# Optimization experiments

Hardware: AMD Instinct MI355X
Metric: run time of the kernel (lower is better)

## Reference

```python
import jax, jax.numpy as jnp
import numpy as np

NUM_HEADS = 16
NEG_INF = -2.0**32 + 1.0  # matches torch code's padding value
LN_EPS = 1e-5


def setup_inputs() -> dict:
    key = jax.random.key(0)
    ks = jax.random.split(key, 4)
    B, S, D = 8, 1024, 1024
    x = jax.random.normal(ks[0], (B, S, D), dtype=jnp.float32)
    W_qkv = jax.random.normal(ks[1], (D, 3 * D), dtype=jnp.float32) * 0.02
    b_qkv = jnp.zeros((3 * D,), dtype=jnp.float32)
    W_out = jax.random.normal(ks[2], (D, D), dtype=jnp.float32) * 0.02
    b_out = jnp.zeros((D,), dtype=jnp.float32)
    gamma = jnp.ones((D,), dtype=jnp.float32)
    beta = jnp.zeros((D,), dtype=jnp.float32)
    return {"x": x, "W_qkv": W_qkv, "b_qkv": b_qkv, "W_out": W_out,
            "b_out": b_out, "gamma": gamma, "beta": beta}


def reference(x, W_qkv, b_qkv, W_out, b_out, gamma, beta):
    B, S, D = x.shape
    H = NUM_HEADS
    hd = D // H
    # fused QKV projection
    qkv = x @ W_qkv + b_qkv                      # [B, S, 3D]
    q, k, v = jnp.split(qkv, 3, axis=-1)         # each [B, S, D]
    # split heads: chunk along feature dim == reshape to [B, H, S, hd]
    q = q.reshape(B, S, H, hd).transpose(0, 2, 1, 3)
    k = k.reshape(B, S, H, hd).transpose(0, 2, 1, 3)
    v = v.reshape(B, S, H, hd).transpose(0, 2, 1, 3)
    # NOTE: original scales by sqrt(num_units), not sqrt(head_dim)
    scale = jnp.float32(1.0 / (D ** 0.5))
    scores = jnp.einsum('bhqd,bhkd->bhqk', q, k) * scale   # [B, H, S, S]
    causal = jnp.tril(jnp.ones((S, S), dtype=bool))
    scores = jnp.where(causal, scores, jnp.float32(NEG_INF))
    attn = jax.nn.softmax(scores, axis=-1)
    o = jnp.einsum('bhqk,bhkd->bhqd', attn, v)             # [B, H, S, hd]
    o = o.transpose(0, 2, 1, 3).reshape(B, S, D)           # concat heads
    out = o @ W_out + b_out + x                            # proj + residual
    # LayerNorm over last dim
    mu = jnp.mean(out, axis=-1, keepdims=True)
    var = jnp.mean((out - mu) ** 2, axis=-1, keepdims=True)
    out = (out - mu) * jax.lax.rsqrt(var + LN_EPS) * gamma + beta
    return out
```

## Files before the change

kernel.cpp:

```cpp
#include <hip/hip_runtime.h>
#include <math.h>

typedef __attribute__((ext_vector_type(8))) short bf16x8;
typedef __attribute__((ext_vector_type(4))) float f32x4;

#define DEV __device__ __forceinline__

DEV unsigned short f2b(float f) {
    union { float f; unsigned u; } x;
    x.f = f;
    unsigned r = x.u + 0x7fff + ((x.u >> 16) & 1);
    return (unsigned short)(r >> 16);
}
DEV float b2f(unsigned short u) {
    union { unsigned u; float f; } x;
    x.u = ((unsigned)u) << 16;
    return x.f;
}

DEV void glds16(const void* g, void* l) {
    __builtin_amdgcn_global_load_lds(
        (const __attribute__((address_space(1))) void*)g,
        (__attribute__((address_space(3))) void*)l, 16, 0, 0);
}

__global__ __launch_bounds__(256) void cvt_bf16(
    const float* __restrict__ in, unsigned short* __restrict__ out)
{
    int i = (blockIdx.x * 256 + threadIdx.x) * 8;
    float4 a = *(const float4*)(in + i);
    float4 b = *(const float4*)(in + i + 4);
    int4 tv;
    short* tp = reinterpret_cast<short*>(&tv);
    tp[0] = (short)f2b(a.x); tp[1] = (short)f2b(a.y);
    tp[2] = (short)f2b(a.z); tp[3] = (short)f2b(a.w);
    tp[4] = (short)f2b(b.x); tp[5] = (short)f2b(b.y);
    tp[6] = (short)f2b(b.z); tp[7] = (short)f2b(b.w);
    *(int4*)(out + i) = tv;
}

__global__ __launch_bounds__(256) void transpose_cvt(
    const float* __restrict__ W, unsigned short* __restrict__ Wt, int N)
{
    __shared__ short S[64 * 65];
    const int n0 = blockIdx.x * 64, k0 = blockIdx.y * 64;
    const int tid = threadIdx.x;
#pragma unroll
    for (int p = 0; p < 16; p++) {
        int idx = p * 256 + tid;
        int r = idx >> 6, c = idx & 63;
        S[c * 65 + r] = (short)f2b(W[(size_t)(k0 + r) * N + n0 + c]);
    }
    __syncthreads();
#pragma unroll
    for (int p = 0; p < 8; p++) {
        int idx = p * 256 + tid;
        int r = idx >> 5, cp = (idx & 31) * 2;
        unsigned lo = (unsigned short)S[r * 65 + cp];
        unsigned hi = (unsigned short)S[r * 65 + cp + 1];
        *(unsigned*)(Wt + (size_t)(n0 + r) * 1024 + k0 + cp) = lo | (hi << 16);
    }
}

__global__ __launch_bounds__(512, 4) void qkv_gemm(
    const unsigned short* __restrict__ Xb,
    const unsigned short* __restrict__ Wt,
    const float* __restrict__ bq,
    unsigned short* __restrict__ Qb,
    unsigned short* __restrict__ Kf,
    unsigned short* __restrict__ Vf)
{
    __shared__ __align__(16) short As[256 * 64];
    __shared__ __align__(16) short Bs[128 * 64];

    const int flat = blockIdx.y * 24 + blockIdx.x;
    const int xcd = flat & 7, local = flat >> 3;
    const int m0 = (xcd * 4 + local / 24) * 256;
    const int n0 = (local % 24) * 128;

    const int tid = threadIdx.x;
    const int wave = tid >> 6, lane = tid & 63;
    const int quad = lane >> 4, lcol = lane & 15;
    const int wr = wave >> 1, wc = wave & 1;
    const int wrow = wr * 64, wcol = wc * 64;

    f32x4 acc[4][4];
#pragma unroll
    for (int i = 0; i < 4; i++)
#pragma unroll
        for (int j = 0; j < 4; j++) acc[i][j] = (f32x4){0.f, 0.f, 0.f, 0.f};

    const int sr = tid >> 3;
    const int g_lin = tid & 7;
    const int g_src = g_lin ^ (sr & 7);
    const int swz = lcol & 7;

    for (int k0 = 0; k0 < 1024; k0 += 64) {
        __syncthreads();
#pragma unroll
        for (int p = 0; p < 4; p++)
            glds16(Xb + (size_t)(m0 + p * 64 + sr) * 1024 + k0 + g_src * 8,
                   &As[(p * 64 + sr) * 64 + g_lin * 8]);
#pragma unroll
        for (int p = 0; p < 2; p++)
            glds16(Wt + (size_t)(n0 + p * 64 + sr) * 1024 + k0 + g_src * 8,
                   &Bs[(p * 64 + sr) * 64 + g_lin * 8]);
        __syncthreads();
#pragma unroll
        for (int kk = 0; kk < 2; kk++) {
            bf16x8 a[4], b[4];
#pragma unroll
            for (int i = 0; i < 4; i++)
                a[i] = *(const bf16x8*)(&As[(wrow + 16 * i + lcol) * 64
                                            + ((kk * 4 + quad) ^ swz) * 8]);
#pragma unroll
            for (int j = 0; j < 4; j++)
                b[j] = *(const bf16x8*)(&Bs[(wcol + 16 * j + lcol) * 64
                                            + ((kk * 4 + quad) ^ swz) * 8]);
#pragma unroll
            for (int i = 0; i < 4; i++)
#pragma unroll
                for (int j = 0; j < 4; j++)
                    acc[i][j] = __builtin_amdgcn_mfma_f32_16x16x32_bf16(
                        a[i], b[j], acc[i][j], 0, 0, 0);
        }
    }
    __syncthreads();

    short* Es = As;
    const int which = n0 >> 10;
    const int h0 = (n0 & 1023) >> 6;
    const int bb = m0 >> 10;
    const int sl0 = m0 & 1023;

#pragma unroll
    for (int hh = 0; hh < 2; hh++) {
        if ((wr >> 1) == hh) {
#pragma unroll
            for (int j = 0; j < 4; j++) {
                int colt = wcol + 16 * j + lcol;
                float bias = bq[n0 + colt];
                int g = colt >> 6, e = colt & 63;
#pragma unroll
                for (int i = 0; i < 4; i++) {
#pragma unroll
                    for (int reg = 0; reg < 4; reg++) {
                        int ls = (wr & 1) * 64 + 16 * i + quad * 4 + reg;
                        unsigned short v = f2b(acc[i][j][reg] + bias);
                        int off;
                        if (which == 0)
                            off = ls * 64 + e;
                        else if (which == 1)
                            off = (e >> 5) * 4096 + (ls >> 4) * 512
                                + (((e >> 3) & 3) * 16 + (ls & 15)) * 8 + (e & 7);
                        else
                            off = (ls >> 5) * 2048 + (e >> 4) * 512
                                + ((((ls >> 3) & 3) * 16) + (e & 15)) * 8 + (ls & 7);
                        Es[g * 8192 + off] = (short)v;
                    }
                }
            }
        }
        __syncthreads();
        const int kt = (sl0 >> 7) + hh;
#pragma unroll
        for (int rd = 0; rd < 4; rd++) {
            int fl = rd * 4096 + tid * 8;
            int g = fl >> 13, off = fl & 8191;
            bf16x8 val = *(const bf16x8*)(&Es[fl]);
            int bh = bb * 16 + h0 + g;
            if (which == 0)
                *(bf16x8*)(Qb + ((size_t)bh * 1024 + sl0 + hh * 128) * 64 + off) = val;
            else if (which == 1)
                *(bf16x8*)(Kf + ((size_t)bh * 8 + kt) * 8192 + off) = val;
            else
                *(bf16x8*)(Vf + ((size_t)bh * 8 + kt) * 8192 + off) = val;
        }
        if (hh == 0) __syncthreads();
    }
}

__global__ __launch_bounds__(256, 4) void attn_kern(
    const unsigned short* __restrict__ Qb,
    const unsigned short* __restrict__ Kf,
    const unsigned short* __restrict__ Vf,
    unsigned short* __restrict__ Ob)
{
    __shared__ __align__(16) short Ps[64 * 136];

    const int xb = blockIdx.x;
    const int bh = blockIdx.y;
    const int pr = xb >> 1;
    const int hf = xb & 1;
    const unsigned short* Qp = Qb + (size_t)bh * 65536;
    const unsigned short* Kp = Kf + (size_t)bh * 65536;
    const unsigned short* Vp = Vf + (size_t)bh * 65536;

    const int tid = threadIdx.x;
    const int wave = tid >> 6, lane = tid & 63;
    const int quad = lane >> 4, lcol = lane & 15;
    const int hw4 = hf * 4 + wave;
    const int qloc = hw4 * 16 + lcol;

    const float sc2 = 0.0450711882f;
    const int b = bh >> 4, h = bh & 15;

    for (int pass = 0; pass < 2; pass++) {
        const int qt = pass ? (7 - pr) : pr;
        const int q0 = qt * 128 + hf * 64 + wave * 16;

        bf16x8 qa[2];
#pragma unroll
        for (int kk = 0; kk < 2; kk++)
            qa[kk] = *(const bf16x8*)(Qp + (size_t)(q0 + lcol) * 64
                                      + kk * 32 + quad * 8);

        f32x4 o_acc[4];
#pragma unroll
        for (int jo = 0; jo < 4; jo++) o_acc[jo] = (f32x4){0.f, 0.f, 0.f, 0.f};
        float l_loc = 0.f;

        for (int kt = 0; kt <= qt; kt++) {
            const bool diag = (kt == qt);
            const int jmax = diag ? hw4 : 7;
            const int kk2max = diag ? (hw4 >> 1) : 3;

            f32x4 scT[8];
#pragma unroll
            for (int j = 0; j < 8; j++) scT[j] = (f32x4){0.f, 0.f, 0.f, 0.f};
#pragma unroll
            for (int kk = 0; kk < 2; kk++) {
                bf16x8 kb[8];
#pragma unroll
                for (int j = 0; j < 8; j++)
                    if (j <= jmax)
                        kb[j] = *(const bf16x8*)(Kp
                            + ((size_t)((kt * 2 + kk) * 8 + j) << 9) + lane * 8);
#pragma unroll
                for (int j = 0; j < 8; j++)
                    if (j <= jmax)
                        scT[j] = __builtin_amdgcn_mfma_f32_16x16x32_bf16(
                            kb[j], qa[kk], scT[j], 0, 0, 0);
            }

#pragma unroll
            for (int j = 0; j < 8; j++) {
                if (j <= jmax) {
                    float pv[4];
#pragma unroll
                    for (int r = 0; r < 4; r++) {
                        float p = exp2f(scT[j][r] * sc2);
                        if (diag && (16 * j + quad * 4 + r) > qloc) p = 0.f;
                        l_loc += p;
                        pv[r] = p;
                    }
                    ushort4 pk;
                    pk.x = f2b(pv[0]); pk.y = f2b(pv[1]);
                    pk.z = f2b(pv[2]); pk.w = f2b(pv[3]);
                    *(ushort4*)(&Ps[(wave * 16 + lcol) * 136 + 16 * j + quad * 4]) = pk;
                }
            }
            if (diag && !(jmax & 1)) {
                *(ushort4*)(&Ps[(wave * 16 + lcol) * 136 + 16 * (jmax + 1) + quad * 4]) =
                    (ushort4){0, 0, 0, 0};
            }

#pragma unroll
            for (int kk2 = 0; kk2 < 4; kk2++) {
                if (kk2 <= kk2max) {
                    bf16x8 pa = *(const bf16x8*)(&Ps[(wave * 16 + lcol) * 136
                                                     + kk2 * 32 + quad * 8]);
                    bf16x8 vb[4];
#pragma unroll
                    for (int jo = 0; jo < 4; jo++)
                        vb[jo] = *(const bf16x8*)(Vp
                            + ((size_t)((kt * 4 + kk2) * 4 + jo) << 9) + lane * 8);
#pragma unroll
                    for (int jo = 0; jo < 4; jo++)
                        o_acc[jo] = __builtin_amdgcn_mfma_f32_16x16x32_bf16(
                            pa, vb[jo], o_acc[jo], 0, 0, 0);
                }
            }
        }

        l_loc += __shfl_xor(l_loc, 16);
        l_loc += __shfl_xor(l_loc, 32);
        float inv = 1.0f / l_loc;
        float invq[4];
#pragma unroll
        for (int r = 0; r < 4; r++) invq[r] = __shfl(inv, quad * 4 + r);

#pragma unroll
        for (int jo = 0; jo < 4; jo++) {
#pragma unroll
            for (int r = 0; r < 4; r++) {
                int q = q0 + quad * 4 + r;
                Ob[(size_t)(b * 1024 + q) * 1024 + h * 64 + 16 * jo + lcol] =
                    f2b(o_acc[jo][r] * invq[r]);
            }
        }
        l_loc = 0.f;
    }
}

__global__ __launch_bounds__(256) void out_gemm(
    const unsigned short* __restrict__ O,
    const unsigned short* __restrict__ Wt2,
    const float* __restrict__ bo,
    const float* __restrict__ X,
    unsigned short* __restrict__ P2)
{
    __shared__ __align__(16) short As[128 * 64];
    __shared__ __align__(16) short Bs[128 * 64];

    const int flat = blockIdx.y * 8 + blockIdx.x;
    const int xcd = flat & 7, local = flat >> 3;
    const int m0 = (xcd * 8 + (local >> 3)) * 128;
    const int n0 = (local & 7) * 128;

    const int tid = threadIdx.x;
    const int wave = tid >> 6, lane = tid & 63;
    const int quad = lane >> 4, lcol = lane & 15;
    const int wrow = (wave >> 1) * 64, wcol = (wave & 1) * 64;

    f32x4 acc[4][4];
#pragma unroll
    for (int i = 0; i < 4; i++)
#pragma unroll
        for (int j = 0; j < 4; j++) acc[i][j] = (f32x4){0.f, 0.f, 0.f, 0.f};

    const int sr = tid >> 3;
    const int g_lin = tid & 7;
    const int g_src = g_lin ^ (sr & 7);
    const int swz = lcol & 7;

    for (int k0 = 0; k0 < 1024; k0 += 64) {
        __syncthreads();
#pragma unroll
        for (int p = 0; p < 4; p++) {
            glds16(O + (size_t)(m0 + p * 32 + sr) * 1024 + k0 + g_src * 8,
                   &As[(p * 32 + sr) * 64 + g_lin * 8]);
            glds16(Wt2 + (size_t)(n0 + p * 32 + sr) * 1024 + k0 + g_src * 8,
                   &Bs[(p * 32 + sr) * 64 + g_lin * 8]);
        }
        __syncthreads();
#pragma unroll
        for (int kk = 0; kk < 2; kk++) {
            bf16x8 a[4], b[4];
#pragma unroll
            for (int i = 0; i < 4; i++)
                a[i] = *(const bf16x8*)(&As[(wrow + 16 * i + lcol) * 64
                                            + ((kk * 4 + quad) ^ swz) * 8]);
#pragma unroll
            for (int j = 0; j < 4; j++)
                b[j] = *(const bf16x8*)(&Bs[(wcol + 16 * j + lcol) * 64
                                            + ((kk * 4 + quad) ^ swz) * 8]);
#pragma unroll
            for (int i = 0; i < 4; i++)
#pragma unroll
                for (int j = 0; j < 4; j++)
                    acc[i][j] = __builtin_amdgcn_mfma_f32_16x16x32_bf16(
                        a[i], b[j], acc[i][j], 0, 0, 0);
        }
    }

#pragma unroll
    for (int j = 0; j < 4; j++) {
        int c = n0 + wcol + 16 * j + lcol;
        float bias = bo[c];
#pragma unroll
        for (int i = 0; i < 4; i++) {
#pragma unroll
            for (int reg = 0; reg < 4; reg++) {
                int r = m0 + wrow + 16 * i + quad * 4 + reg;
                float v = acc[i][j][reg] + bias + X[(size_t)r * 1024 + c];
                P2[(size_t)r * 1024 + c] = f2b(v);
            }
        }
    }
}

__global__ __launch_bounds__(256) void ln_kern(
    const unsigned short* __restrict__ P2,
    const float* __restrict__ G,
    const float* __restrict__ Bt,
    float* __restrict__ out)
{
    const int row = blockIdx.x, tid = threadIdx.x;
    const size_t base = (size_t)row * 1024 + tid * 4;

    int2 raw = *(const int2*)(P2 + base);
    float v[4];
    v[0] = b2f((unsigned short)(raw.x & 0xffff));
    v[1] = b2f((unsigned short)((unsigned)raw.x >> 16));
    v[2] = b2f((unsigned short)(raw.y & 0xffff));
    v[3] = b2f((unsigned short)((unsigned)raw.y >> 16));

    float sum = v[0] + v[1] + v[2] + v[3];
    float sq = v[0] * v[0] + v[1] * v[1] + v[2] * v[2] + v[3] * v[3];
#pragma unroll
    for (int m = 1; m < 64; m <<= 1) {
        sum += __shfl_xor(sum, m);
        sq += __shfl_xor(sq, m);
    }
    __shared__ float rs[4], rq[4];
    const int wave = tid >> 6, lane = tid & 63;
    if (lane == 0) { rs[wave] = sum; rq[wave] = sq; }
    __syncthreads();
    sum = rs[0] + rs[1] + rs[2] + rs[3];
    sq = rq[0] + rq[1] + rq[2] + rq[3];

    float mean = sum * (1.0f / 1024.0f);
    float var = fmaxf(sq * (1.0f / 1024.0f) - mean * mean, 0.0f);
    float rstd = rsqrtf(var + 1e-5f);

    float4 g = *(const float4*)(G + tid * 4);
    float4 be = *(const float4*)(Bt + tid * 4);

    float4 o;
    o.x = (v[0] - mean) * rstd * g.x + be.x;
    o.y = (v[1] - mean) * rstd * g.y + be.y;
    o.z = (v[2] - mean) * rstd * g.z + be.z;
    o.w = (v[3] - mean) * rstd * g.w + be.w;
    *(float4*)(out + base) = o;
}

extern "C" void kernel_launch(void* const* d_in, const int* in_sizes, int n_in,
                              void* d_out, int out_size, void* d_ws, size_t ws_size,
                              hipStream_t stream) {
    const float* x    = (const float*)d_in[0];
    const float* Wqkv = (const float*)d_in[1];
    const float* bqkv = (const float*)d_in[2];
    const float* Wout = (const float*)d_in[3];
    const float* bout = (const float*)d_in[4];
    const float* gam  = (const float*)d_in[5];
    const float* bet  = (const float*)d_in[6];
    float* out = (float*)d_out;

    char* ws = (char*)d_ws;
    const size_t MB = (size_t)1024 * 1024;

    unsigned short* Qb  = (unsigned short*)d_out;
    unsigned short* Ob  = (unsigned short*)d_out + 8388608;
    unsigned short* Kf  = (unsigned short*)(ws);
    unsigned short* Vf  = (unsigned short*)(ws + 16 * MB);
    unsigned short* Wt2 = (unsigned short*)(ws + 32 * MB);
    unsigned short* Xb  = (unsigned short*)(ws + 34 * MB);
    unsigned short* Wt  = (unsigned short*)(ws + 50 * MB);
    unsigned short* P2  = (unsigned short*)(ws + 34 * MB);

    cvt_bf16<<<4096, 256, 0, stream>>>(x, Xb);
    transpose_cvt<<<dim3(48, 16), 256, 0, stream>>>(Wqkv, Wt, 3072);
    transpose_cvt<<<dim3(16, 16), 256, 0, stream>>>(Wout, Wt2, 1024);
    qkv_gemm<<<dim3(24, 32), 512, 0, stream>>>(Xb, Wt, bqkv, Qb, Kf, Vf);
    attn_kern<<<dim3(8, 128), 256, 0, stream>>>(Qb, Kf, Vf, Ob);
    out_gemm<<<dim3(8, 64), 256, 0, stream>>>(Ob, Wt2, bout, x, P2);
    ln_kern<<<8192, 256, 0, stream>>>(P2, gam, bet, out);
}
```

Baseline: 292.0 us.

## Merge prep kernels into one launch, add MFMA priority hints, relax qkv launch bounds

Folds the input bf16 conversion and both weight transpose-converts into a single prep kernel, dispatching on block index, which saves two kernel launches and their tail gaps. Wraps the MFMA bursts in the attention kernel with s_setprio raise/lower so waves issuing matrix ops are favoured over waves doing softmax and loads. Drops the min-blocks hint from qkv_gemm's launch bounds, so the compiler has more registers to use per thread but occupancy may fall. The prep kernel now has divergent block roles and keeps shared memory allocated even for the conversion blocks.

```diff
diff --git a/kernel.cpp b/kernel.cpp
--- a/kernel.cpp
+++ b/kernel.cpp
@@ -24,27 +24,40 @@
         (__attribute__((address_space(3))) void*)l, 16, 0, 0);
 }
 
-__global__ __launch_bounds__(256) void cvt_bf16(
-    const float* __restrict__ in, unsigned short* __restrict__ out)
-{
-    int i = (blockIdx.x * 256 + threadIdx.x) * 8;
-    float4 a = *(const float4*)(in + i);
-    float4 b = *(const float4*)(in + i + 4);
-    int4 tv;
-    short* tp = reinterpret_cast<short*>(&tv);
-    tp[0] = (short)f2b(a.x); tp[1] = (short)f2b(a.y);
-    tp[2] = (short)f2b(a.z); tp[3] = (short)f2b(a.w);
-    tp[4] = (short)f2b(b.x); tp[5] = (short)f2b(b.y);
-    tp[6] = (short)f2b(b.z); tp[7] = (short)f2b(b.w);
-    *(int4*)(out + i) = tv;
-}
-
-__global__ __launch_bounds__(256) void transpose_cvt(
-    const float* __restrict__ W, unsigned short* __restrict__ Wt, int N)
+__global__ __launch_bounds__(256) void prep_kern(
+    const float* __restrict__ x,    unsigned short* __restrict__ Xb,
+    const float* __restrict__ Wqkv, unsigned short* __restrict__ Wt,
+    const float* __restrict__ Wout, unsigned short* __restrict__ Wt2)
 {
     __shared__ short S[64 * 65];
-    const int n0 = blockIdx.x * 64, k0 = blockIdx.y * 64;
-    const int tid = threadIdx.x;
+    const int id = blockIdx.x, tid = threadIdx.x;
+
+    if (id < 4096) {
+        int i = (id * 256 + tid) * 8;
+        float4 a = *(const float4*)(x + i);
+        float4 b = *(const float4*)(x + i + 4);
+        int4 tv;
+        short* tp = reinterpret_cast<short*>(&tv);
+        tp[0] = (short)f2b(a.x); tp[1] = (short)f2b(a.y);
+        tp[2] = (short)f2b(a.z); tp[3] = (short)f2b(a.w);
+        tp[4] = (short)f2b(b.x); tp[5] = (short)f2b(b.y);
+        tp[6] = (short)f2b(b.z); tp[7] = (short)f2b(b.w);
+        *(int4*)(Xb + i) = tv;
+        return;
+    }
+
+    const float* W;
+    unsigned short* Wo;
+    int N, n0, k0;
+    if (id < 4864) {
+        int t = id - 4096;
+        W = Wqkv; Wo = Wt; N = 3072;
+        n0 = (t % 48) * 64; k0 = (t / 48) * 64;
+    } else {
+        int t = id - 4864;
+        W = Wout; Wo = Wt2; N = 1024;
+        n0 = (t % 16) * 64; k0 = (t / 16) * 64;
+    }
 #pragma unroll
     for (int p = 0; p < 16; p++) {
         int idx = p * 256 + tid;
@@ -58,11 +71,11 @@
         int r = idx >> 5, cp = (idx & 31) * 2;
         unsigned lo = (unsigned short)S[r * 65 + cp];
         unsigned hi = (unsigned short)S[r * 65 + cp + 1];
-        *(unsigned*)(Wt + (size_t)(n0 + r) * 1024 + k0 + cp) = lo | (hi << 16);
-    }
-}
-
-__global__ __launch_bounds__(512, 4) void qkv_gemm(
+        *(unsigned*)(Wo + (size_t)(n0 + r) * 1024 + k0 + cp) = lo | (hi << 16);
+    }
+}
+
+__global__ __launch_bounds__(512) void qkv_gemm(
     const unsigned short* __restrict__ Xb,
     const unsigned short* __restrict__ Wt,
     const float* __restrict__ bq,
@@ -236,11 +249,13 @@
                     if (j <= jmax)
                         kb[j] = *(const bf16x8*)(Kp
                             + ((size_t)((kt * 2 + kk) * 8 + j) << 9) + lane * 8);
+                __builtin_amdgcn_s_setprio(1);
 #pragma unroll
                 for (int j = 0; j < 8; j++)
                     if (j <= jmax)
                         scT[j] = __builtin_amdgcn_mfma_f32_16x16x32_bf16(
                             kb[j], qa[kk], scT[j], 0, 0, 0);
+                __builtin_amdgcn_s_setprio(0);
             }
 
 #pragma unroll
@@ -275,10 +290,12 @@
                     for (int jo = 0; jo < 4; jo++)
                         vb[jo] = *(const bf16x8*)(Vp
                             + ((size_t)((kt * 4 + kk2) * 4 + jo) << 9) + lane * 8);
+                    __builtin_amdgcn_s_setprio(1);
 #pragma unroll
                     for (int jo = 0; jo < 4; jo++)
                         o_acc[jo] = __builtin_amdgcn_mfma_f32_16x16x32_bf16(
                             pa, vb[jo], o_acc[jo], 0, 0, 0);
+                    __builtin_amdgcn_s_setprio(0);
                 }
             }
         }
@@ -449,9 +466,7 @@
     unsigned short* Wt  = (unsigned short*)(ws + 50 * MB);
     unsigned short* P2  = (unsigned short*)(ws + 34 * MB);
 
-    cvt_bf16<<<4096, 256, 0, stream>>>(x, Xb);
-    transpose_cvt<<<dim3(48, 16), 256, 0, stream>>>(Wqkv, Wt, 3072);
-    transpose_cvt<<<dim3(16, 16), 256, 0, stream>>>(Wout, Wt2, 1024);
+    prep_kern<<<5120, 256, 0, stream>>>(x, Xb, Wqkv, Wt, Wout, Wt2);
     qkv_gemm<<<dim3(24, 32), 512, 0, stream>>>(Xb, Wt, bqkv, Qb, Kf, Vf);
     attn_kern<<<dim3(8, 128), 256, 0, stream>>>(Qb, Kf, Vf, Ob);
     out_gemm<<<dim3(8, 64), 256, 0, stream>>>(Ob, Wt2, bout, x, P2);
```

Result: faster. 279.1 us (-4.4%).
